# Kernel tuning notes

Hardware: AMD Instinct MI355X
Metric: run time of the kernel (lower is better)

Reference implementation:

```python
import jax, jax.numpy as jnp
import numpy as np

HIDDEN = 1024
NUM_HEADS = 16
HEAD_DIM = HIDDEN // NUM_HEADS


def setup_inputs() -> dict:
    key = jax.random.key(0)
    ks = jax.random.split(key, 11)
    s = 1.0 / np.sqrt(HIDDEN)
    x = jax.random.normal(ks[0], (4, 2048, HIDDEN), dtype=jnp.float32)
    Wq = jax.random.uniform(ks[1], (HIDDEN, HIDDEN), jnp.float32, -s, s)
    bq = jax.random.uniform(ks[2], (HIDDEN,), jnp.float32, -s, s)
    Wk = jax.random.uniform(ks[3], (HIDDEN, HIDDEN), jnp.float32, -s, s)
    bk = jax.random.uniform(ks[4], (HIDDEN,), jnp.float32, -s, s)
    Wv = jax.random.uniform(ks[5], (HIDDEN, HIDDEN), jnp.float32, -s, s)
    bv = jax.random.uniform(ks[6], (HIDDEN,), jnp.float32, -s, s)
    Wo = jax.random.uniform(ks[7], (HIDDEN, HIDDEN), jnp.float32, -s, s)
    bo = jax.random.uniform(ks[8], (HIDDEN,), jnp.float32, -s, s)
    ln_g = jnp.ones((HIDDEN,), jnp.float32)
    ln_b = jnp.zeros((HIDDEN,), jnp.float32)
    return {"x": x, "Wq": Wq, "bq": bq, "Wk": Wk, "bk": bk,
            "Wv": Wv, "bv": bv, "Wo": Wo, "bo": bo,
            "ln_g": ln_g, "ln_b": ln_b}


def _layer_norm(x, g, b, eps=1e-5):
    mu = jnp.mean(x, axis=-1, keepdims=True)
    var = jnp.var(x, axis=-1, keepdims=True)
    return (x - mu) * jax.lax.rsqrt(var + eps) * g + b


def reference(x, Wq, bq, Wk, bk, Wv, bv, Wo, bo, ln_g, ln_b):
    B, S, _ = x.shape
    residual = x
    h = _layer_norm(x, ln_g, ln_b)
    # projections (torch Linear: y = h @ W.T + b)
    q = (h @ Wq.T + bq).reshape(B, S, NUM_HEADS, HEAD_DIM).transpose(0, 2, 1, 3)
    k = (h @ Wk.T + bk).reshape(B, S, NUM_HEADS, HEAD_DIM).transpose(0, 2, 1, 3)
    v = (h @ Wv.T + bv).reshape(B, S, NUM_HEADS, HEAD_DIM).transpose(0, 2, 1, 3)
    scores = jnp.einsum('bhqd,bhkd->bhqk', q, k) / np.sqrt(HEAD_DIM).astype(np.float32)
    weights = jax.nn.softmax(scores, axis=-1)  # dropout = identity (eval mode)
    context = jnp.einsum('bhqk,bhkd->bhqd', weights, v)
    context = context.transpose(0, 2, 1, 3).reshape(B, S, HIDDEN)
    out = context @ Wo.T + bo
    return out + residual
```

## Files before the change

kernel.cpp:

```cpp
#include <hip/hip_runtime.h>

typedef unsigned short u16;
typedef unsigned int   u32;
using bf16x8 = __attribute__((ext_vector_type(8))) __bf16;
using f32x4  = __attribute__((ext_vector_type(4))) float;
using u32x2  = __attribute__((ext_vector_type(2))) unsigned int;

__device__ __forceinline__ float b2f(u16 u){ union { float f; u32 i; } v; v.i = ((u32)u) << 16; return v.f; }
__device__ __forceinline__ u16 f2b(float f){
  union { float f; u32 i; } v; v.f = f;
  u32 r = v.i + 0x7FFFu + ((v.i >> 16) & 1u);
  return (u16)(r >> 16);
}
__device__ __forceinline__ u32 pk_bf16_trunc(float a, float b){
  return __builtin_amdgcn_perm(__float_as_uint(b), __float_as_uint(a), 0x07060302u);
}

__global__ __launch_bounds__(256) void cvt_w(const float* __restrict__ s0, const float* __restrict__ s1,
                                             const float* __restrict__ s2, const float* __restrict__ s3,
                                             u16* __restrict__ d){
  const float* srcs[4] = {s0, s1, s2, s3};
  const float* s = srcs[blockIdx.y];
  u16* dd = d + (size_t)blockIdx.y * (1024u * 1024u);
  const int i = (blockIdx.x * 256 + threadIdx.x) * 4;
  float4 v = *(const float4*)(s + i);
  uint2 o;
  o.x = (u32)f2b(v.x) | ((u32)f2b(v.y) << 16);
  o.y = (u32)f2b(v.z) | ((u32)f2b(v.w) << 16);
  *(uint2*)(dd + i) = o;
}

__global__ __launch_bounds__(256) void ln_kernel(const float* __restrict__ x, const float* __restrict__ g,
                                                 const float* __restrict__ be, u16* __restrict__ h){
  const int row = blockIdx.x, tid = threadIdx.x;
  const float* xr = x + (size_t)row * 1024u;
  float4 raw = *(const float4*)(xr + tid * 4);
  float s  = raw.x + raw.y + raw.z + raw.w;
  float sq = raw.x*raw.x + raw.y*raw.y + raw.z*raw.z + raw.w*raw.w;
  #pragma unroll
  for (int m = 1; m < 64; m <<= 1){ s += __shfl_xor(s, m); sq += __shfl_xor(sq, m); }
  __shared__ float ws[4], wq[4];
  if ((tid & 63) == 0){ ws[tid >> 6] = s; wq[tid >> 6] = sq; }
  __syncthreads();
  s  = ws[0] + ws[1] + ws[2] + ws[3];
  sq = wq[0] + wq[1] + wq[2] + wq[3];
  const float mu = s * (1.0f / 1024.0f);
  const float rstd = rsqrtf(sq * (1.0f / 1024.0f) - mu * mu + 1e-5f);
  float4 gg = *(const float4*)(g + tid * 4);
  float4 bb = *(const float4*)(be + tid * 4);
  float y0 = (raw.x - mu) * rstd * gg.x + bb.x;
  float y1 = (raw.y - mu) * rstd * gg.y + bb.y;
  float y2 = (raw.z - mu) * rstd * gg.z + bb.z;
  float y3 = (raw.w - mu) * rstd * gg.w + bb.w;
  uint2 outv;
  outv.x = (u32)f2b(y0) | ((u32)f2b(y1) << 16);
  outv.y = (u32)f2b(y2) | ((u32)f2b(y3) << 16);
  *(uint2*)(h + (size_t)row * 1024u + tid * 4) = outv;
}

__global__ __launch_bounds__(256) void gemm_qkv(const u16* __restrict__ A, const u16* __restrict__ Wcat,
                                                const float* __restrict__ bq, const float* __restrict__ bk,
                                                const float* __restrict__ bv,
                                                u16* __restrict__ qo, u16* __restrict__ ko, u16* __restrict__ vo){
  __shared__ u16 lA[128 * 32];
  __shared__ u16 lB[128 * 32];
  const int tid = threadIdx.x;
  const int lane = tid & 63, wv = tid >> 6, l15 = lane & 15, quad = lane >> 4;
  const int wr = wv >> 1, wc = wv & 1;
  const int row0 = blockIdx.x * 128, col0 = blockIdx.y * 128;
  const int K = 1024;
  f32x4 acc[4][4] = {};
  for (int kt = 0; kt < 32; ++kt){
    __syncthreads();
    #pragma unroll
    for (int jj = 0; jj < 2; ++jj){
      int idx = jj * 256 + tid;
      int r = idx >> 2, c = idx & 3;
      __builtin_amdgcn_global_load_lds(
        (const __attribute__((address_space(1))) void*)(A + (size_t)(row0 + r) * K + (kt * 32 + c * 8)),
        (__attribute__((address_space(3))) void*)(&lA[idx * 8]), 16, 0, 0);
      __builtin_amdgcn_global_load_lds(
        (const __attribute__((address_space(1))) void*)(Wcat + (size_t)(col0 + r) * K + (kt * 32 + c * 8)),
        (__attribute__((address_space(3))) void*)(&lB[idx * 8]), 16, 0, 0);
    }
    __syncthreads();
    bf16x8 af[4], bf[4];
    #pragma unroll
    for (int i = 0; i < 4; ++i) af[i] = *(const bf16x8*)&lA[(wr * 64 + i * 16 + l15) * 32 + quad * 8];
    #pragma unroll
    for (int j = 0; j < 4; ++j) bf[j] = *(const bf16x8*)&lB[(wc * 64 + j * 16 + l15) * 32 + quad * 8];
    #pragma unroll
    for (int i = 0; i < 4; ++i)
      #pragma unroll
      for (int j = 0; j < 4; ++j)
        acc[i][j] = __builtin_amdgcn_mfma_f32_16x16x32_bf16(af[i], bf[j], acc[i][j], 0, 0, 0);
  }
  const int sel = col0 >> 10;
  const float* bias = (sel == 0) ? bq : (sel == 1) ? bk : bv;
  u16* dst = (sel == 0) ? qo : (sel == 1) ? ko : vo;
  #pragma unroll
  for (int i = 0; i < 4; ++i){
    const int grow = row0 + wr * 64 + i * 16 + quad * 4;
    #pragma unroll
    for (int j = 0; j < 4; ++j){
      const int gcol = (col0 & 1023) + wc * 64 + j * 16 + l15;
      const float bb = bias[gcol];
      #pragma unroll
      for (int r = 0; r < 4; ++r){
        size_t off = (size_t)(grow + r) * 1024u + gcol;
        dst[off] = f2b(acc[i][j][r] + bb);
      }
    }
  }
}

__global__ __launch_bounds__(256) void gemm_out(const u16* __restrict__ A, const u16* __restrict__ W,
                                                const float* __restrict__ bias, const float* __restrict__ res,
                                                float* __restrict__ C, int M, int N, int K){
  __shared__ u16 lA[128 * 32];
  __shared__ u16 lB[128 * 32];
  const int tid = threadIdx.x;
  const int lane = tid & 63, wv = tid >> 6, l15 = lane & 15, quad = lane >> 4;
  const int wr = wv >> 1, wc = wv & 1;
  const int row0 = blockIdx.x * 128, col0 = blockIdx.y * 128;
  f32x4 acc[4][4] = {};
  const int nkt = K >> 5;
  for (int kt = 0; kt < nkt; ++kt){
    __syncthreads();
    #pragma unroll
    for (int jj = 0; jj < 2; ++jj){
      int idx = jj * 256 + tid;
      int r = idx >> 2, c = idx & 3;
      __builtin_amdgcn_global_load_lds(
        (const __attribute__((address_space(1))) void*)(A + (size_t)(row0 + r) * K + (kt * 32 + c * 8)),
        (__attribute__((address_space(3))) void*)(&lA[idx * 8]), 16, 0, 0);
      __builtin_amdgcn_global_load_lds(
        (const __attribute__((address_space(1))) void*)(W + (size_t)(col0 + r) * K + (kt * 32 + c * 8)),
        (__attribute__((address_space(3))) void*)(&lB[idx * 8]), 16, 0, 0);
    }
    __syncthreads();
    bf16x8 af[4], bf[4];
    #pragma unroll
    for (int i = 0; i < 4; ++i) af[i] = *(const bf16x8*)&lA[(wr * 64 + i * 16 + l15) * 32 + quad * 8];
    #pragma unroll
    for (int j = 0; j < 4; ++j) bf[j] = *(const bf16x8*)&lB[(wc * 64 + j * 16 + l15) * 32 + quad * 8];
    #pragma unroll
    for (int i = 0; i < 4; ++i)
      #pragma unroll
      for (int j = 0; j < 4; ++j)
        acc[i][j] = __builtin_amdgcn_mfma_f32_16x16x32_bf16(af[i], bf[j], acc[i][j], 0, 0, 0);
  }
  #pragma unroll
  for (int i = 0; i < 4; ++i){
    const int grow = row0 + wr * 64 + i * 16 + quad * 4;
    #pragma unroll
    for (int j = 0; j < 4; ++j){
      const int gcol = col0 + wc * 64 + j * 16 + l15;
      const float bb = bias[gcol];
      #pragma unroll
      for (int r = 0; r < 4; ++r){
        size_t off = (size_t)(grow + r) * N + gcol;
        C[off] = acc[i][j][r] + bb + res[off];
      }
    }
  }
}

__global__ __launch_bounds__(256) void transpose_v(const u16* __restrict__ V, u16* __restrict__ Vt){
  __shared__ u16 t[64 * 66];
  const int bh = blockIdx.x >> 5, st = blockIdx.x & 31;
  const int b = bh >> 4, hh = bh & 15;
  const u16* Vg = V + ((size_t)b * 2048u + st * 64u) * 1024u + hh * 64;
  u16* Og = Vt + (size_t)bh * 64u * 2048u + st * 64u;
  #pragma unroll
  for (int i = 0; i < 16; ++i){
    int idx = i * 256 + threadIdx.x;
    int s = idx >> 6, d = idx & 63;
    t[s * 66 + d] = Vg[(size_t)s * 1024u + d];
  }
  __syncthreads();
  #pragma unroll
  for (int i = 0; i < 16; ++i){
    int idx = i * 256 + threadIdx.x;
    int d = idx >> 6, s = idx & 63;
    Og[(size_t)d * 2048u + s] = t[s * 66 + d];
  }
}

__global__ __launch_bounds__(256, 4) void attn_kernel(const u16* __restrict__ Q, const u16* __restrict__ K,
                                                      const u16* __restrict__ Vt, u16* __restrict__ O){
  __shared__ u16 kls[2][64 * 64];
  __shared__ u16 vls[2][64 * 64];
  const int tid = threadIdx.x;
  const int lane = tid & 63, wv = tid >> 6, l15 = lane & 15, quad = lane >> 4;
  const int bh = blockIdx.x & 63, qt = blockIdx.x >> 6;
  const int b = bh >> 4, hh = bh & 15;
  const int q0 = qt * 128;
  const u16* Qg = Q + ((size_t)b * 2048u) * 1024u + hh * 64;
  const u16* Kg = K + ((size_t)b * 2048u) * 1024u + hh * 64;
  const u16* Vg = Vt + (size_t)bh * 64u * 2048u;
  u16* Og = O + ((size_t)b * 2048u) * 1024u + hh * 64;

  const int sr = tid >> 3, sc = tid & 7, sr2 = sr + 32;
  const int sx = (sc ^ (sr & 7)) * 8;
  const int c0 = ((quad ^ (l15 & 7))) * 8;

  const float QSCALE = 0.125f * 1.44269504f;
  bf16x8 qf2[2][2];
  #pragma unroll
  for (int g = 0; g < 2; ++g)
    #pragma unroll
    for (int kk = 0; kk < 2; ++kk){
      qf2[g][kk] = *(const bf16x8*)(Qg + (size_t)(q0 + wv * 32 + g * 16 + l15) * 1024u + kk * 32 + quad * 8);
      #pragma unroll
      for (int e = 0; e < 8; ++e) qf2[g][kk][e] = (__bf16)((float)qf2[g][kk][e] * QSCALE);
    }

  bf16x8 ones_f;
  {
    const __bf16 onev = (__bf16)1.0f, zerov = (__bf16)0.0f;
    #pragma unroll
    for (int e = 0; e < 8; ++e) ones_f[e] = (l15 == 0) ? onev : zerov;
  }

  f32x4 o2[2][4] = {};
  f32x4 o_l[2] = {};
  const f32x4 zf = {0.f, 0.f, 0.f, 0.f};

  uint4 kr0, kr1, vr0, vr1;
  kr0 = *(const uint4*)(Kg + (size_t)sr  * 1024u + sc * 8);
  vr0 = *(const uint4*)(Vg + (size_t)sr  * 2048u + sc * 8);
  kr1 = *(const uint4*)(Kg + (size_t)sr2 * 1024u + sc * 8);
  vr1 = *(const uint4*)(Vg + (size_t)sr2 * 2048u + sc * 8);
  *(uint4*)&kls[0][sr  * 64 + sx] = kr0;
  *(uint4*)&vls[0][sr  * 64 + sx] = vr0;
  *(uint4*)&kls[0][sr2 * 64 + sx] = kr1;
  *(uint4*)&vls[0][sr2 * 64 + sx] = vr1;
  kr0 = *(const uint4*)(Kg + (size_t)(64 + sr)  * 1024u + sc * 8);
  vr0 = *(const uint4*)(Vg + (size_t)sr  * 2048u + 64 + sc * 8);
  kr1 = *(const uint4*)(Kg + (size_t)(64 + sr2) * 1024u + sc * 8);
  vr1 = *(const uint4*)(Vg + (size_t)sr2 * 2048u + 64 + sc * 8);
  __syncthreads();

  for (int kt = 0; kt < 32; ++kt){
    const int cur = kt & 1;
    const u16* kb = kls[cur];
    const u16* vb = vls[cur];
    if (kt < 31){
      u16* kw = kls[cur ^ 1];
      u16* vw = vls[cur ^ 1];
      *(uint4*)&kw[sr  * 64 + sx] = kr0;
      *(uint4*)&vw[sr  * 64 + sx] = vr0;
      *(uint4*)&kw[sr2 * 64 + sx] = kr1;
      *(uint4*)&vw[sr2 * 64 + sx] = vr1;
    }
    if (kt < 30){
      const int s0 = (kt + 2) * 64;
      kr0 = *(const uint4*)(Kg + (size_t)(s0 + sr)  * 1024u + sc * 8);
      vr0 = *(const uint4*)(Vg + (size_t)sr  * 2048u + s0 + sc * 8);
      kr1 = *(const uint4*)(Kg + (size_t)(s0 + sr2) * 1024u + sc * 8);
      vr1 = *(const uint4*)(Vg + (size_t)sr2 * 2048u + s0 + sc * 8);
    }

    f32x4 s2[2][4];
    #pragma unroll
    for (int j = 0; j < 4; ++j){
      const int rb = (j * 16 + l15) * 64;
      bf16x8 kfr0 = *(const bf16x8*)&kb[rb + c0];
      bf16x8 kfr1 = *(const bf16x8*)&kb[rb + (c0 ^ 32)];
      #pragma unroll
      for (int g = 0; g < 2; ++g){
        f32x4 a = __builtin_amdgcn_mfma_f32_16x16x32_bf16(kfr0, qf2[g][0], zf, 0, 0, 0);
        s2[g][j] = __builtin_amdgcn_mfma_f32_16x16x32_bf16(kfr1, qf2[g][1], a, 0, 0, 0);
      }
    }

    #pragma unroll
    for (int g = 0; g < 2; ++g)
      #pragma unroll
      for (int j = 0; j < 4; ++j)
        #pragma unroll
        for (int r = 0; r < 4; ++r)
          s2[g][j][r] = __builtin_amdgcn_exp2f(s2[g][j][r]);

    #pragma unroll
    for (int kk = 0; kk < 2; ++kk){
      bf16x8 afr[2];
      #pragma unroll
      for (int g = 0; g < 2; ++g){
        const int j0 = kk * 2, j1 = j0 + 1;
        u32 A0 = pk_bf16_trunc(s2[g][j0][0], s2[g][j0][1]);
        u32 A1 = pk_bf16_trunc(s2[g][j0][2], s2[g][j0][3]);
        u32 B0 = pk_bf16_trunc(s2[g][j1][0], s2[g][j1][1]);
        u32 B1 = pk_bf16_trunc(s2[g][j1][2], s2[g][j1][3]);
        u32x2 r1 = __builtin_amdgcn_permlane32_swap(A0, B0, false, false);
        u32x2 r2 = __builtin_amdgcn_permlane16_swap(r1[0], r1[1], false, false);
        u32x2 r3 = __builtin_amdgcn_permlane32_swap(A1, B1, false, false);
        u32x2 r4 = __builtin_amdgcn_permlane16_swap(r3[0], r3[1], false, false);
        union { uint4 u; bf16x8 v; } cv;
        cv.u.x = r2[0]; cv.u.y = r4[0]; cv.u.z = r2[1]; cv.u.w = r4[1];
        afr[g] = cv.v;
      }
      #pragma unroll
      for (int g = 0; g < 2; ++g)
        o_l[g] = __builtin_amdgcn_mfma_f32_16x16x32_bf16(afr[g], ones_f, o_l[g], 0, 0, 0);
      #pragma unroll
      for (int j2 = 0; j2 < 4; ++j2){
        bf16x8 bfr = *(const bf16x8*)&vb[(j2 * 16 + l15) * 64 + (c0 ^ (kk * 32))];
        #pragma unroll
        for (int g = 0; g < 2; ++g)
          o2[g][j2] = __builtin_amdgcn_mfma_f32_16x16x32_bf16(afr[g], bfr, o2[g][j2], 0, 0, 0);
      }
    }
    __syncthreads();
  }

  #pragma unroll
  for (int g = 0; g < 2; ++g){
    float lr[4];
    #pragma unroll
    for (int r = 0; r < 4; ++r) lr[r] = 1.0f / __shfl(o_l[g][r], quad * 16);
    #pragma unroll
    for (int j2 = 0; j2 < 4; ++j2){
      #pragma unroll
      for (int r = 0; r < 4; ++r){
        const int qrow = q0 + wv * 32 + g * 16 + quad * 4 + r;
        const int d = j2 * 16 + l15;
        Og[(size_t)qrow * 1024u + d] = f2b(o2[g][j2][r] * lr[r]);
      }
    }
  }
}

extern "C" void kernel_launch(void* const* d_in, const int* in_sizes, int n_in,
                              void* d_out, int out_size, void* d_ws, size_t ws_size,
                              hipStream_t stream){
  (void)in_sizes; (void)n_in; (void)out_size; (void)ws_size;
  const float* x   = (const float*)d_in[0];
  const float* Wq  = (const float*)d_in[1];
  const float* bq  = (const float*)d_in[2];
  const float* Wk  = (const float*)d_in[3];
  const float* bk  = (const float*)d_in[4];
  const float* Wv  = (const float*)d_in[5];
  const float* bv  = (const float*)d_in[6];
  const float* Wo  = (const float*)d_in[7];
  const float* bo  = (const float*)d_in[8];
  const float* lng = (const float*)d_in[9];
  const float* lnb = (const float*)d_in[10];
  float* out = (float*)d_out;

  const size_t TE = (size_t)8192 * 1024;
  u16* ws0 = (u16*)d_ws;
  u16* ws1 = ws0 + TE;
  u16* ws2 = ws1 + TE;
  u16* wsw = ws2 + TE;
  u16* wob = wsw + (size_t)3 * 1024 * 1024;
  u16* v   = (u16*)d_out;

  cvt_w<<<dim3(1024, 4), 256, 0, stream>>>(Wq, Wk, Wv, Wo, wsw);
  ln_kernel<<<dim3(8192), 256, 0, stream>>>(x, lng, lnb, ws0);
  gemm_qkv<<<dim3(64, 24), 256, 0, stream>>>(ws0, wsw, bq, bk, bv, ws1, ws2, v);
  transpose_v<<<dim3(2048), 256, 0, stream>>>(v, ws0);
  attn_kernel<<<dim3(1024), 256, 0, stream>>>(ws1, ws2, ws0, ws1);
  gemm_out<<<dim3(64, 8), 256, 0, stream>>>(ws1, wob, bo, x, out, 8192, 1024, 1024);
}
```

Baseline: 287.7 us.

## Replace QKV and output GEMMs with double-buffered 8-wave pipelined GEMM

Both GEMMs now use one templated kernel with 512 threads, 128x256 tiles and BK=64. LDS is double-buffered with XOR-swizzled layouts to avoid bank conflicts, and global-to-LDS loads are interleaved with MFMA phases using manual barriers, waitcnt and setprio. Blocks are remapped for L2 locality. The aim is to hide load latency and raise MFMA utilisation, at the cost of fragile hand-scheduled synchronisation and higher LDS use per block.

```diff
diff --git a/kernel.cpp b/kernel.cpp
--- a/kernel.cpp
+++ b/kernel.cpp
@@ -58,112 +58,147 @@
   *(uint2*)(h + (size_t)row * 1024u + tid * 4) = outv;
 }
 
-__global__ __launch_bounds__(256) void gemm_qkv(const u16* __restrict__ A, const u16* __restrict__ Wcat,
-                                                const float* __restrict__ bq, const float* __restrict__ bk,
-                                                const float* __restrict__ bv,
-                                                u16* __restrict__ qo, u16* __restrict__ ko, u16* __restrict__ vo){
-  __shared__ u16 lA[128 * 32];
-  __shared__ u16 lB[128 * 32];
+#define GLL(gp, lp) __builtin_amdgcn_global_load_lds( \
+    (const __attribute__((address_space(1))) void*)(gp), \
+    (__attribute__((address_space(3))) void*)(lp), 16, 0, 0)
+
+template<int MODE>
+__global__ __launch_bounds__(512, 1) void gemm8p(const u16* __restrict__ A, const u16* __restrict__ W,
+    const float* __restrict__ bq, const float* __restrict__ bk, const float* __restrict__ bv,
+    const float* __restrict__ res, u16* __restrict__ qo, u16* __restrict__ ko, u16* __restrict__ vo,
+    float* __restrict__ oc){
+  __shared__ u16 lA[2][128 * 64];
+  __shared__ u16 lB[2][256 * 64];
   const int tid = threadIdx.x;
   const int lane = tid & 63, wv = tid >> 6, l15 = lane & 15, quad = lane >> 4;
-  const int wr = wv >> 1, wc = wv & 1;
-  const int row0 = blockIdx.x * 128, col0 = blockIdx.y * 128;
-  const int K = 1024;
+  const int wr = wv >> 2, wc = wv & 3;
+  const int nwg = gridDim.x;
+  const int f0 = blockIdx.x;
+  const int wg = (f0 & 7) * (nwg >> 3) + (f0 >> 3);
+  const int mtile = wg & 63, ntile = wg >> 6;
+  const int row0 = mtile * 128, col0 = ntile * 256;
+
+  const int srow = tid >> 3;
+  const int scs  = (tid & 7) ^ (srow & 7);
+  const u16* Asrc = A + (size_t)(row0 + srow) * 1024u + scs * 8;
+  const u16* Bsrc = W + (size_t)(col0 + srow) * 1024u + scs * 8;
+
+  const int ck0 = (quad ^ (l15 & 7)) * 8;
+  const int ck1 = ((quad + 4) ^ (l15 & 7)) * 8;
+  const int arow = wr * 64 + l15;
+  const int brow = wc * 64 + l15;
+
   f32x4 acc[4][4] = {};
-  for (int kt = 0; kt < 32; ++kt){
-    __syncthreads();
-    #pragma unroll
-    for (int jj = 0; jj < 2; ++jj){
-      int idx = jj * 256 + tid;
-      int r = idx >> 2, c = idx & 3;
-      __builtin_amdgcn_global_load_lds(
-        (const __attribute__((address_space(1))) void*)(A + (size_t)(row0 + r) * K + (kt * 32 + c * 8)),
-        (__attribute__((address_space(3))) void*)(&lA[idx * 8]), 16, 0, 0);
-      __builtin_amdgcn_global_load_lds(
-        (const __attribute__((address_space(1))) void*)(Wcat + (size_t)(col0 + r) * K + (kt * 32 + c * 8)),
-        (__attribute__((address_space(3))) void*)(&lB[idx * 8]), 16, 0, 0);
-    }
-    __syncthreads();
-    bf16x8 af[4], bf[4];
-    #pragma unroll
-    for (int i = 0; i < 4; ++i) af[i] = *(const bf16x8*)&lA[(wr * 64 + i * 16 + l15) * 32 + quad * 8];
-    #pragma unroll
-    for (int j = 0; j < 4; ++j) bf[j] = *(const bf16x8*)&lB[(wc * 64 + j * 16 + l15) * 32 + quad * 8];
-    #pragma unroll
-    for (int i = 0; i < 4; ++i)
-      #pragma unroll
-      for (int j = 0; j < 4; ++j)
-        acc[i][j] = __builtin_amdgcn_mfma_f32_16x16x32_bf16(af[i], bf[j], acc[i][j], 0, 0, 0);
-  }
-  const int sel = col0 >> 10;
-  const float* bias = (sel == 0) ? bq : (sel == 1) ? bk : bv;
-  u16* dst = (sel == 0) ? qo : (sel == 1) ? ko : vo;
-  #pragma unroll
-  for (int i = 0; i < 4; ++i){
-    const int grow = row0 + wr * 64 + i * 16 + quad * 4;
-    #pragma unroll
-    for (int j = 0; j < 4; ++j){
-      const int gcol = (col0 & 1023) + wc * 64 + j * 16 + l15;
-      const float bb = bias[gcol];
-      #pragma unroll
-      for (int r = 0; r < 4; ++r){
-        size_t off = (size_t)(grow + r) * 1024u + gcol;
-        dst[off] = f2b(acc[i][j][r] + bb);
-      }
-    }
-  }
-}
-
-__global__ __launch_bounds__(256) void gemm_out(const u16* __restrict__ A, const u16* __restrict__ W,
-                                                const float* __restrict__ bias, const float* __restrict__ res,
-                                                float* __restrict__ C, int M, int N, int K){
-  __shared__ u16 lA[128 * 32];
-  __shared__ u16 lB[128 * 32];
-  const int tid = threadIdx.x;
-  const int lane = tid & 63, wv = tid >> 6, l15 = lane & 15, quad = lane >> 4;
-  const int wr = wv >> 1, wc = wv & 1;
-  const int row0 = blockIdx.x * 128, col0 = blockIdx.y * 128;
-  f32x4 acc[4][4] = {};
-  const int nkt = K >> 5;
-  for (int kt = 0; kt < nkt; ++kt){
-    __syncthreads();
-    #pragma unroll
-    for (int jj = 0; jj < 2; ++jj){
-      int idx = jj * 256 + tid;
-      int r = idx >> 2, c = idx & 3;
-      __builtin_amdgcn_global_load_lds(
-        (const __attribute__((address_space(1))) void*)(A + (size_t)(row0 + r) * K + (kt * 32 + c * 8)),
-        (__attribute__((address_space(3))) void*)(&lA[idx * 8]), 16, 0, 0);
-      __builtin_amdgcn_global_load_lds(
-        (const __attribute__((address_space(1))) void*)(W + (size_t)(col0 + r) * K + (kt * 32 + c * 8)),
-        (__attribute__((address_space(3))) void*)(&lB[idx * 8]), 16, 0, 0);
-    }
-    __syncthreads();
-    bf16x8 af[4], bf[4];
-    #pragma unroll
-    for (int i = 0; i < 4; ++i) af[i] = *(const bf16x8*)&lA[(wr * 64 + i * 16 + l15) * 32 + quad * 8];
-    #pragma unroll
-    for (int j = 0; j < 4; ++j) bf[j] = *(const bf16x8*)&lB[(wc * 64 + j * 16 + l15) * 32 + quad * 8];
-    #pragma unroll
-    for (int i = 0; i < 4; ++i)
-      #pragma unroll
-      for (int j = 0; j < 4; ++j)
-        acc[i][j] = __builtin_amdgcn_mfma_f32_16x16x32_bf16(af[i], bf[j], acc[i][j], 0, 0, 0);
-  }
-  #pragma unroll
-  for (int i = 0; i < 4; ++i){
-    const int grow = row0 + wr * 64 + i * 16 + quad * 4;
-    #pragma unroll
-    for (int j = 0; j < 4; ++j){
-      const int gcol = col0 + wc * 64 + j * 16 + l15;
-      const float bb = bias[gcol];
-      #pragma unroll
-      for (int r = 0; r < 4; ++r){
-        size_t off = (size_t)(grow + r) * N + gcol;
-        C[off] = acc[i][j][r] + bb + res[off];
-      }
-    }
-  }
+  bf16x8 a00, a01, a10, a11, b00, b01, b10, b11, b20, b21, b30, b31;
+
+#define STAGE_A(bufi, kt) do{ const u16* s_ = Asrc + (kt) * 64; \
+    GLL(s_,              &lA[bufi][tid * 8]); \
+    GLL(s_ + 64 * 1024u, &lA[bufi][(512 + tid) * 8]); }while(0)
+#define STAGE_B(bufi, kt) do{ const u16* s_ = Bsrc + (kt) * 64; \
+    GLL(s_,               &lB[bufi][tid * 8]); \
+    GLL(s_ +  64 * 1024u, &lB[bufi][( 512 + tid) * 8]); \
+    GLL(s_ + 128 * 1024u, &lB[bufi][(1024 + tid) * 8]); \
+    GLL(s_ + 192 * 1024u, &lB[bufi][(1536 + tid) * 8]); }while(0)
+#define LDSA(bufi, m, kk) (*(const bf16x8*)&lA[bufi][(arow + (m) * 16) * 64 + ((kk) ? ck1 : ck0)])
+#define LDSB(bufi, n, kk) (*(const bf16x8*)&lB[bufi][(brow + (n) * 16) * 64 + ((kk) ? ck1 : ck0)])
+#define READS_FULL(bufi, M0, M1) \
+    a00 = LDSA(bufi, M0, 0); a01 = LDSA(bufi, M0, 1); \
+    a10 = LDSA(bufi, M1, 0); a11 = LDSA(bufi, M1, 1); \
+    b00 = LDSB(bufi, 0, 0);  b01 = LDSB(bufi, 0, 1); \
+    b10 = LDSB(bufi, 1, 0);  b11 = LDSB(bufi, 1, 1); \
+    b20 = LDSB(bufi, 2, 0);  b21 = LDSB(bufi, 2, 1); \
+    b30 = LDSB(bufi, 3, 0);  b31 = LDSB(bufi, 3, 1);
+#define READS_A(bufi, M0, M1) \
+    a00 = LDSA(bufi, M0, 0); a01 = LDSA(bufi, M0, 1); \
+    a10 = LDSA(bufi, M1, 0); a11 = LDSA(bufi, M1, 1);
+#define MFMA(d, a, b) d = __builtin_amdgcn_mfma_f32_16x16x32_bf16(a, b, d, 0, 0, 0)
+#define PHASE_MFMA(I0, I1) \
+    __builtin_amdgcn_s_setprio(1); \
+    MFMA(acc[I0][0], a00, b00); MFMA(acc[I1][0], a10, b00); \
+    MFMA(acc[I0][1], a00, b10); MFMA(acc[I1][1], a10, b10); \
+    MFMA(acc[I0][2], a00, b20); MFMA(acc[I1][2], a10, b20); \
+    MFMA(acc[I0][3], a00, b30); MFMA(acc[I1][3], a10, b30); \
+    MFMA(acc[I0][0], a01, b01); MFMA(acc[I1][0], a11, b01); \
+    MFMA(acc[I0][1], a01, b11); MFMA(acc[I1][1], a11, b11); \
+    MFMA(acc[I0][2], a01, b21); MFMA(acc[I1][2], a11, b21); \
+    MFMA(acc[I0][3], a01, b31); MFMA(acc[I1][3], a11, b31); \
+    __builtin_amdgcn_s_setprio(0);
+#define PH_MID() do{ asm volatile("s_barrier" ::: "memory"); \
+    asm volatile("s_waitcnt lgkmcnt(0)" ::: "memory"); \
+    __builtin_amdgcn_sched_barrier(0); }while(0)
+#define PH_END() asm volatile("s_barrier" ::: "memory")
+#define PH_END_VM() do{ asm volatile("s_waitcnt vmcnt(4)" ::: "memory"); \
+    asm volatile("s_barrier" ::: "memory"); }while(0)
+
+  STAGE_A(0, 0); STAGE_B(0, 0); STAGE_B(1, 1);
+  asm volatile("s_waitcnt vmcnt(4)" ::: "memory");
+  asm volatile("s_barrier" ::: "memory");
+
+  #pragma unroll 1
+  for (int i = 0; i < 8; ++i){
+    const int t1 = 2 * i + 1;
+    const int t2 = (2 * i + 2 > 15) ? 15 : 2 * i + 2;
+    const int t3 = (2 * i + 3 > 15) ? 15 : 2 * i + 3;
+    READS_FULL(0, 0, 1);
+    STAGE_A(1, t1);
+    PH_MID(); PHASE_MFMA(0, 1); PH_END();
+    READS_A(0, 2, 3);
+    STAGE_B(0, t2);
+    PH_MID(); PHASE_MFMA(2, 3); PH_END_VM();
+    READS_FULL(1, 0, 1);
+    STAGE_A(0, t2);
+    PH_MID(); PHASE_MFMA(0, 1); PH_END();
+    READS_A(1, 2, 3);
+    STAGE_B(1, t3);
+    PH_MID(); PHASE_MFMA(2, 3); PH_END_VM();
+  }
+  asm volatile("s_waitcnt vmcnt(0)" ::: "memory");
+
+  if (MODE == 0){
+    const int sel = col0 >> 10;
+    const float* bias = (sel == 0) ? bq : (sel == 1) ? bk : bv;
+    u16* dst = (sel == 0) ? qo : (sel == 1) ? ko : vo;
+    const int colbase = (col0 & 1023) + wc * 64;
+    #pragma unroll
+    for (int m = 0; m < 4; ++m){
+      const int grow = row0 + wr * 64 + m * 16 + quad * 4;
+      #pragma unroll
+      for (int n = 0; n < 4; ++n){
+        const int gcol = colbase + n * 16 + l15;
+        const float bb = bias[gcol];
+        #pragma unroll
+        for (int r = 0; r < 4; ++r)
+          dst[(size_t)(grow + r) * 1024u + gcol] = f2b(acc[m][n][r] + bb);
+      }
+    }
+  } else {
+    const int colbase = col0 + wc * 64;
+    #pragma unroll
+    for (int m = 0; m < 4; ++m){
+      const int grow = row0 + wr * 64 + m * 16 + quad * 4;
+      #pragma unroll
+      for (int n = 0; n < 4; ++n){
+        const int gcol = colbase + n * 16 + l15;
+        const float bb = bq[gcol];
+        #pragma unroll
+        for (int r = 0; r < 4; ++r){
+          size_t off = (size_t)(grow + r) * 1024u + gcol;
+          oc[off] = acc[m][n][r] + bb + res[off];
+        }
+      }
+    }
+  }
+#undef STAGE_A
+#undef STAGE_B
+#undef LDSA
+#undef LDSB
+#undef READS_FULL
+#undef READS_A
+#undef MFMA
+#undef PHASE_MFMA
+#undef PH_MID
+#undef PH_END
+#undef PH_END_VM
 }
 
 __global__ __launch_bounds__(256) void transpose_v(const u16* __restrict__ V, u16* __restrict__ Vt){
@@ -359,8 +394,8 @@
 
   cvt_w<<<dim3(1024, 4), 256, 0, stream>>>(Wq, Wk, Wv, Wo, wsw);
   ln_kernel<<<dim3(8192), 256, 0, stream>>>(x, lng, lnb, ws0);
-  gemm_qkv<<<dim3(64, 24), 256, 0, stream>>>(ws0, wsw, bq, bk, bv, ws1, ws2, v);
+  gemm8p<0><<<dim3(768), 512, 0, stream>>>(ws0, wsw, bq, bk, bv, nullptr, ws1, ws2, v, nullptr);
   transpose_v<<<dim3(2048), 256, 0, stream>>>(v, ws0);
   attn_kernel<<<dim3(1024), 256, 0, stream>>>(ws1, ws2, ws0, ws1);
-  gemm_out<<<dim3(64, 8), 256, 0, stream>>>(ws1, wob, bo, x, out, 8192, 1024, 1024);
-}
+  gemm8p<1><<<dim3(256), 512, 0, stream>>>(ws1, wob, bo, nullptr, nullptr, x, nullptr, nullptr, nullptr, out);
+}
```

After: 297.0 us. +3.2%, slower.

## Fuse V transpose into QKV GEMM epilogue and double attention query tile

Applied to the files above, without the earlier changes.

The QKV GEMM epilogue now writes V directly in per-head transposed layout (packed 4-element stores along sequence), which removes the separate transpose_v kernel and its extra read/write pass. Separately, each attention block now handles 256 query rows (64 per wave) instead of 128, halving the grid and reusing every loaded K/V tile across twice as many queries. The larger per-wave accumulator set raises register pressure, so the occupancy hint drops from 4 to 2 blocks per CU, which may reduce latency hiding. Attention occupancy also falls to 512 blocks.

```diff
diff --git a/kernel.cpp b/kernel.cpp
--- a/kernel.cpp
+++ b/kernel.cpp
@@ -6,7 +6,6 @@
 using f32x4  = __attribute__((ext_vector_type(4))) float;
 using u32x2  = __attribute__((ext_vector_type(2))) unsigned int;
 
-__device__ __forceinline__ float b2f(u16 u){ union { float f; u32 i; } v; v.i = ((u32)u) << 16; return v.f; }
 __device__ __forceinline__ u16 f2b(float f){
   union { float f; u32 i; } v; v.f = f;
   u32 r = v.i + 0x7FFFu + ((v.i >> 16) & 1u);
@@ -61,7 +60,7 @@
 __global__ __launch_bounds__(256) void gemm_qkv(const u16* __restrict__ A, const u16* __restrict__ Wcat,
                                                 const float* __restrict__ bq, const float* __restrict__ bk,
                                                 const float* __restrict__ bv,
-                                                u16* __restrict__ qo, u16* __restrict__ ko, u16* __restrict__ vo){
+                                                u16* __restrict__ qo, u16* __restrict__ ko, u16* __restrict__ vt){
   __shared__ u16 lA[128 * 32];
   __shared__ u16 lB[128 * 32];
   const int tid = threadIdx.x;
@@ -96,19 +95,37 @@
         acc[i][j] = __builtin_amdgcn_mfma_f32_16x16x32_bf16(af[i], bf[j], acc[i][j], 0, 0, 0);
   }
   const int sel = col0 >> 10;
-  const float* bias = (sel == 0) ? bq : (sel == 1) ? bk : bv;
-  u16* dst = (sel == 0) ? qo : (sel == 1) ? ko : vo;
-  #pragma unroll
-  for (int i = 0; i < 4; ++i){
-    const int grow = row0 + wr * 64 + i * 16 + quad * 4;
-    #pragma unroll
-    for (int j = 0; j < 4; ++j){
-      const int gcol = (col0 & 1023) + wc * 64 + j * 16 + l15;
-      const float bb = bias[gcol];
-      #pragma unroll
-      for (int r = 0; r < 4; ++r){
-        size_t off = (size_t)(grow + r) * 1024u + gcol;
-        dst[off] = f2b(acc[i][j][r] + bb);
+  if (sel < 2){
+    const float* bias = (sel == 0) ? bq : bk;
+    u16* dst = (sel == 0) ? qo : ko;
+    #pragma unroll
+    for (int i = 0; i < 4; ++i){
+      const int grow = row0 + wr * 64 + i * 16 + quad * 4;
+      #pragma unroll
+      for (int j = 0; j < 4; ++j){
+        const int gcol = (col0 & 1023) + wc * 64 + j * 16 + l15;
+        const float bb = bias[gcol];
+        #pragma unroll
+        for (int r = 0; r < 4; ++r){
+          size_t off = (size_t)(grow + r) * 1024u + gcol;
+          dst[off] = f2b(acc[i][j][r] + bb);
+        }
+      }
+    }
+  } else {
+    #pragma unroll
+    for (int i = 0; i < 4; ++i){
+      const int grow = row0 + wr * 64 + i * 16 + quad * 4;
+      const int bb_  = grow >> 11, srem = grow & 2047;
+      #pragma unroll
+      for (int j = 0; j < 4; ++j){
+        const int gcol = (col0 & 1023) + wc * 64 + j * 16 + l15;
+        const int head = gcol >> 6, d = gcol & 63;
+        const float bv_ = bv[gcol];
+        uint2 pk;
+        pk.x = (u32)f2b(acc[i][j][0] + bv_) | ((u32)f2b(acc[i][j][1] + bv_) << 16);
+        pk.y = (u32)f2b(acc[i][j][2] + bv_) | ((u32)f2b(acc[i][j][3] + bv_) << 16);
+        *(uint2*)(vt + ((size_t)((bb_ * 16 + head) * 64 + d)) * 2048u + srem) = pk;
       }
     }
   }
@@ -166,28 +183,7 @@
   }
 }
 
-__global__ __launch_bounds__(256) void transpose_v(const u16* __restrict__ V, u16* __restrict__ Vt){
-  __shared__ u16 t[64 * 66];
-  const int bh = blockIdx.x >> 5, st = blockIdx.x & 31;
-  const int b = bh >> 4, hh = bh & 15;
-  const u16* Vg = V + ((size_t)b * 2048u + st * 64u) * 1024u + hh * 64;
-  u16* Og = Vt + (size_t)bh * 64u * 2048u + st * 64u;
-  #pragma unroll
-  for (int i = 0; i < 16; ++i){
-    int idx = i * 256 + threadIdx.x;
-    int s = idx >> 6, d = idx & 63;
-    t[s * 66 + d] = Vg[(size_t)s * 1024u + d];
-  }
-  __syncthreads();
-  #pragma unroll
-  for (int i = 0; i < 16; ++i){
-    int idx = i * 256 + threadIdx.x;
-    int d = idx >> 6, s = idx & 63;
-    Og[(size_t)d * 2048u + s] = t[s * 66 + d];
-  }
-}
-
-__global__ __launch_bounds__(256, 4) void attn_kernel(const u16* __restrict__ Q, const u16* __restrict__ K,
+__global__ __launch_bounds__(256, 2) void attn_kernel(const u16* __restrict__ Q, const u16* __restrict__ K,
                                                       const u16* __restrict__ Vt, u16* __restrict__ O){
   __shared__ u16 kls[2][64 * 64];
   __shared__ u16 vls[2][64 * 64];
@@ -195,7 +191,7 @@
   const int lane = tid & 63, wv = tid >> 6, l15 = lane & 15, quad = lane >> 4;
   const int bh = blockIdx.x & 63, qt = blockIdx.x >> 6;
   const int b = bh >> 4, hh = bh & 15;
-  const int q0 = qt * 128;
+  const int q0 = qt * 256;
   const u16* Qg = Q + ((size_t)b * 2048u) * 1024u + hh * 64;
   const u16* Kg = K + ((size_t)b * 2048u) * 1024u + hh * 64;
   const u16* Vg = Vt + (size_t)bh * 64u * 2048u;
@@ -206,12 +202,12 @@
   const int c0 = ((quad ^ (l15 & 7))) * 8;
 
   const float QSCALE = 0.125f * 1.44269504f;
-  bf16x8 qf2[2][2];
+  bf16x8 qf2[4][2];
   #pragma unroll
-  for (int g = 0; g < 2; ++g)
+  for (int g = 0; g < 4; ++g)
     #pragma unroll
     for (int kk = 0; kk < 2; ++kk){
-      qf2[g][kk] = *(const bf16x8*)(Qg + (size_t)(q0 + wv * 32 + g * 16 + l15) * 1024u + kk * 32 + quad * 8);
+      qf2[g][kk] = *(const bf16x8*)(Qg + (size_t)(q0 + wv * 64 + g * 16 + l15) * 1024u + kk * 32 + quad * 8);
       #pragma unroll
       for (int e = 0; e < 8; ++e) qf2[g][kk][e] = (__bf16)((float)qf2[g][kk][e] * QSCALE);
     }
@@ -223,8 +219,8 @@
     for (int e = 0; e < 8; ++e) ones_f[e] = (l15 == 0) ? onev : zerov;
   }
 
-  f32x4 o2[2][4] = {};
-  f32x4 o_l[2] = {};
+  f32x4 o2[4][4] = {};
+  f32x4 o_l[4] = {};
   const f32x4 zf = {0.f, 0.f, 0.f, 0.f};
 
   uint4 kr0, kr1, vr0, vr1;
@@ -262,21 +258,21 @@
       vr1 = *(const uint4*)(Vg + (size_t)sr2 * 2048u + s0 + sc * 8);
     }
 
-    f32x4 s2[2][4];
+    f32x4 s2[4][4];
     #pragma unroll
     for (int j = 0; j < 4; ++j){
       const int rb = (j * 16 + l15) * 64;
       bf16x8 kfr0 = *(const bf16x8*)&kb[rb + c0];
       bf16x8 kfr1 = *(const bf16x8*)&kb[rb + (c0 ^ 32)];
       #pragma unroll
-      for (int g = 0; g < 2; ++g){
+      for (int g = 0; g < 4; ++g){
         f32x4 a = __builtin_amdgcn_mfma_f32_16x16x32_bf16(kfr0, qf2[g][0], zf, 0, 0, 0);
         s2[g][j] = __builtin_amdgcn_mfma_f32_16x16x32_bf16(kfr1, qf2[g][1], a, 0, 0, 0);
       }
     }
 
     #pragma unroll
-    for (int g = 0; g < 2; ++g)
+    for (int g = 0; g < 4; ++g)
       #pragma unroll
       for (int j = 0; j < 4; ++j)
         #pragma unroll
@@ -285,9 +281,9 @@
 
     #pragma unroll
     for (int kk = 0; kk < 2; ++kk){
-      bf16x8 afr[2];
-      #pragma unroll
-      for (int g = 0; g < 2; ++g){
+      bf16x8 afr[4];
+      #pragma unroll
+      for (int g = 0; g < 4; ++g){
         const int j0 = kk * 2, j1 = j0 + 1;
         u32 A0 = pk_bf16_trunc(s2[g][j0][0], s2[g][j0][1]);
         u32 A1 = pk_bf16_trunc(s2[g][j0][2], s2[g][j0][3]);
@@ -302,13 +298,13 @@
         afr[g] = cv.v;
       }
       #pragma unroll
-      for (int g = 0; g < 2; ++g)
+      for (int g = 0; g < 4; ++g)
         o_l[g] = __builtin_amdgcn_mfma_f32_16x16x32_bf16(afr[g], ones_f, o_l[g], 0, 0, 0);
       #pragma unroll
       for (int j2 = 0; j2 < 4; ++j2){
         bf16x8 bfr = *(const bf16x8*)&vb[(j2 * 16 + l15) * 64 + (c0 ^ (kk * 32))];
         #pragma unroll
-        for (int g = 0; g < 2; ++g)
+        for (int g = 0; g < 4; ++g)
           o2[g][j2] = __builtin_amdgcn_mfma_f32_16x16x32_bf16(afr[g], bfr, o2[g][j2], 0, 0, 0);
       }
     }
@@ -316,7 +312,7 @@
   }
 
   #pragma unroll
-  for (int g = 0; g < 2; ++g){
+  for (int g = 0; g < 4; ++g){
     float lr[4];
     #pragma unroll
     for (int r = 0; r < 4; ++r) lr[r] = 1.0f / __shfl(o_l[g][r], quad * 16);
@@ -324,7 +320,7 @@
     for (int j2 = 0; j2 < 4; ++j2){
       #pragma unroll
       for (int r = 0; r < 4; ++r){
-        const int qrow = q0 + wv * 32 + g * 16 + quad * 4 + r;
+        const int qrow = q0 + wv * 64 + g * 16 + quad * 4 + r;
         const int d = j2 * 16 + l15;
         Og[(size_t)qrow * 1024u + d] = f2b(o2[g][j2][r] * lr[r]);
       }
@@ -355,12 +351,11 @@
   u16* ws2 = ws1 + TE;
   u16* wsw = ws2 + TE;
   u16* wob = wsw + (size_t)3 * 1024 * 1024;
-  u16* v   = (u16*)d_out;
+  u16* vt  = (u16*)d_out;
 
   cvt_w<<<dim3(1024, 4), 256, 0, stream>>>(Wq, Wk, Wv, Wo, wsw);
   ln_kernel<<<dim3(8192), 256, 0, stream>>>(x, lng, lnb, ws0);
-  gemm_qkv<<<dim3(64, 24), 256, 0, stream>>>(ws0, wsw, bq, bk, bv, ws1, ws2, v);
-  transpose_v<<<dim3(2048), 256, 0, stream>>>(v, ws0);
-  attn_kernel<<<dim3(1024), 256, 0, stream>>>(ws1, ws2, ws0, ws1);
+  gemm_qkv<<<dim3(64, 24), 256, 0, stream>>>(ws0, wsw, bq, bk, bv, ws1, ws2, vt);
+  attn_kernel<<<dim3(512), 256, 0, stream>>>(ws1, ws2, vt, ws1);
   gemm_out<<<dim3(64, 8), 256, 0, stream>>>(ws1, wob, bo, x, out, 8192, 1024, 1024);
 }
```

Result: faster. 279.3 us (-2.9%).
